# Kernel optimization log

Hardware: AMD Instinct MI355X
Metric: run time of the kernel (lower is better)

Reference implementation:

```python
import jax, jax.numpy as jnp
import numpy as np

N_NODES = 100000
N_EDGES = 20000  # hyperedges
NNZ = 800000
D = 128


def setup_inputs() -> dict:
    key = jax.random.key(0)
    ks = jax.random.split(key, 10)
    X = jax.random.normal(ks[0], (N_NODES, D), dtype=jnp.float32)
    X0 = jax.random.normal(ks[1], (N_NODES, D), dtype=jnp.float32)
    degE = jax.random.uniform(ks[2], (N_EDGES, 1), dtype=jnp.float32)
    degV = jax.random.uniform(ks[3], (N_NODES, 1), dtype=jnp.float32)
    alpha = jax.random.uniform(ks[4], (1,), dtype=jnp.float32)
    beta = jax.random.uniform(ks[5], (1,), dtype=jnp.float32)
    W_w = jax.random.normal(ks[6], (D, D), dtype=jnp.float32) / np.sqrt(D)
    g1_src = jax.random.randint(ks[7], (NNZ,), 0, N_NODES, dtype=jnp.int64 if jax.config.read('jax_enable_x64') else jnp.int32)
    g1_dst = jax.random.randint(ks[8], (NNZ,), 0, N_EDGES)
    g2_src = jax.random.randint(ks[9], (NNZ,), 0, N_EDGES)
    g2_dst = jax.random.randint(jax.random.fold_in(key, 99), (NNZ,), 0, N_NODES)
    return {"X": X, "X0": X0, "degE": degE, "degV": degV, "alpha": alpha,
            "beta": beta, "W_w": W_w, "g1_src": g1_src, "g1_dst": g1_dst,
            "g2_src": g2_src, "g2_dst": g2_dst}


def reference(X, X0, degE, degV, alpha, beta, W_w, g1_src, g1_dst, g2_src, g2_dst):
    n_edges = degE.shape[0]
    n_nodes = degV.shape[0]
    a = alpha[0]
    b = beta[0]
    # copy_u_sum(g1, X): gather node rows, scatter-sum into hyperedges
    Xe = jax.ops.segment_sum(X[g1_src], g1_dst, num_segments=n_edges)  # [E, D]
    Xe = Xe * degE
    # copy_u_sum(g2, Xe): gather hyperedge rows, scatter-sum into nodes
    Xv = jax.ops.segment_sum(Xe[g2_src], g2_dst, num_segments=n_nodes)  # [N, D]
    Xv = Xv * degV
    # GCNII-style initial residual + identity mapping
    Xi = (1.0 - a) * Xv + a * X0
    out = (1.0 - b) * Xi + b * (Xi @ W_w.T)  # Linear(bias=False)
    return out
```

## Files before the change

kernel.cpp:

```cpp
#include <hip/hip_runtime.h>

#define DD 128
#define SCAN_CHUNK 2048
#define PAD1 16
#define PAD2 8

typedef __attribute__((ext_vector_type(8))) _Float16 f16x8;
typedef __attribute__((ext_vector_type(4))) _Float16 f16x4;
typedef __attribute__((ext_vector_type(4))) float f32x4;

__global__ __launch_bounds__(256)
void k_hist1(const int* __restrict__ g1d, int* __restrict__ cnt1p,
             int* __restrict__ rank1, int nnz, int no, int hb,
             const float* __restrict__ W, const float* __restrict__ betaP,
             _Float16* __restrict__ Mh,
             const float* __restrict__ X, _Float16* __restrict__ Xh, int nx) {
    const int b = blockIdx.x;
    if (b < hb) {
        int q = b * 256 + threadIdx.x;
        if (q >= no) return;
        int i = q << 3;
        if (i + 8 <= nnz) {
            int4 d0 = *(const int4*)(g1d + i);
            int4 d1 = *(const int4*)(g1d + i + 4);
            int r0 = atomicAdd(&cnt1p[d0.x * PAD1], 1);
            int r1 = atomicAdd(&cnt1p[d0.y * PAD1], 1);
            int r2 = atomicAdd(&cnt1p[d0.z * PAD1], 1);
            int r3 = atomicAdd(&cnt1p[d0.w * PAD1], 1);
            int r4 = atomicAdd(&cnt1p[d1.x * PAD1], 1);
            int r5 = atomicAdd(&cnt1p[d1.y * PAD1], 1);
            int r6 = atomicAdd(&cnt1p[d1.z * PAD1], 1);
            int r7 = atomicAdd(&cnt1p[d1.w * PAD1], 1);
            *(int4*)(rank1 + i)     = make_int4(r0, r1, r2, r3);
            *(int4*)(rank1 + i + 4) = make_int4(r4, r5, r6, r7);
        } else {
            for (; i < nnz; ++i) rank1[i] = atomicAdd(&cnt1p[g1d[i] * PAD1], 1);
        }
        return;
    }
    if (b < hb + 8) {
        int gid = (b - hb) * 256 + threadIdx.x;
        if (gid >= DD * DD / 8) return;
        int c  = gid >> 4;
        int k0 = (gid & 15) << 3;
        float bb = betaP[0], ib = 1.0f - bb;
        const float* p = W + c * DD + k0;
        float4 lo = *(const float4*)p, hi = *(const float4*)(p + 4);
        float v[8] = {lo.x, lo.y, lo.z, lo.w, hi.x, hi.y, hi.z, hi.w};
        f16x8 t;
        #pragma unroll
        for (int j = 0; j < 8; ++j) {
            float m = bb * v[j] + ((k0 + j) == c ? ib : 0.0f);
            t[j] = (_Float16)m;
        }
        *(f16x8*)(Mh + (size_t)c * DD + k0) = t;
        return;
    }
    int gid = (b - hb - 8) * 256 + threadIdx.x;
    int i = gid << 3;
    if (i + 8 <= nx) {
        float4 lo = *(const float4*)(X + i);
        float4 hi = *(const float4*)(X + i + 4);
        f16x8 t;
        t[0] = (_Float16)lo.x; t[1] = (_Float16)lo.y;
        t[2] = (_Float16)lo.z; t[3] = (_Float16)lo.w;
        t[4] = (_Float16)hi.x; t[5] = (_Float16)hi.y;
        t[6] = (_Float16)hi.z; t[7] = (_Float16)hi.w;
        *(f16x8*)(Xh + i) = t;
    } else {
        for (; i < nx; ++i) Xh[i] = (_Float16)X[i];
    }
}

__global__ __launch_bounds__(256)
void k_scan_blocks(const int* __restrict__ cnt, int* __restrict__ off,
                   int* __restrict__ bsum, int n, int str) {
    __shared__ int sh[256];
    const int tid = threadIdx.x;
    const int base = blockIdx.x * SCAN_CHUNK + tid * 8;
    int v[8];
    int s = 0;
    #pragma unroll
    for (int j = 0; j < 8; ++j) {
        int idx = base + j;
        v[j] = (idx < n) ? cnt[(size_t)idx * str] : 0;
        s += v[j];
    }
    sh[tid] = s;
    __syncthreads();
    for (int d = 1; d < 256; d <<= 1) {
        int y = (tid >= d) ? sh[tid - d] : 0;
        __syncthreads();
        sh[tid] += y;
        __syncthreads();
    }
    int incl = sh[tid];
    int run = incl - s;
    #pragma unroll
    for (int j = 0; j < 8; ++j) {
        int idx = base + j;
        if (idx <= n) off[idx] = run;
        run += v[j];
    }
    if (tid == 255) bsum[blockIdx.x] = incl;
}

__global__ __launch_bounds__(256)
void k_fill(const int* __restrict__ dst, const int* __restrict__ src,
            const int* __restrict__ off, const int* __restrict__ rank,
            const int* __restrict__ bsum, int nb,
            int* __restrict__ out, int nnz) {
    __shared__ int pref[64];
    if (threadIdx.x == 0) {
        int run = 0;
        for (int i = 0; i < nb; ++i) { pref[i] = run; run += bsum[i]; }
        pref[nb] = run;
    }
    __syncthreads();
    int q = blockIdx.x * 256 + threadIdx.x;
    int i = q << 2;
    if (i + 4 <= nnz) {
        int4 d = *(const int4*)(dst + i);
        int4 s = *(const int4*)(src + i);
        int4 r = *(const int4*)(rank + i);
        int o0 = off[d.x] + pref[d.x >> 11];
        int o1 = off[d.y] + pref[d.y >> 11];
        int o2 = off[d.z] + pref[d.z >> 11];
        int o3 = off[d.w] + pref[d.w >> 11];
        out[o0 + r.x] = s.x;
        out[o1 + r.y] = s.y;
        out[o2 + r.z] = s.z;
        out[o3 + r.w] = s.w;
    } else {
        for (; i < nnz; ++i)
            out[off[dst[i]] + pref[dst[i] >> 11] + rank[i]] = src[i];
    }
}

__global__ __launch_bounds__(256)
void k_h2_egather(const int* __restrict__ g2d, int* __restrict__ cnt2p,
                  int* __restrict__ rank2, int nnz, int no, int H,
                  const _Float16* __restrict__ Xh, const int* __restrict__ off1,
                  const int* __restrict__ bsum1, int nb1,
                  const int* __restrict__ srcs1, const float* __restrict__ degE,
                  _Float16* __restrict__ XeH, int n_edges) {
    if (blockIdx.x < H) {
        int q = blockIdx.x * 256 + threadIdx.x;
        if (q >= no) return;
        int i = q << 3;
        if (i + 8 <= nnz) {
            int4 d0 = *(const int4*)(g2d + i);
            int4 d1 = *(const int4*)(g2d + i + 4);
            int r0 = atomicAdd(&cnt2p[d0.x * PAD2], 1);
            int r1 = atomicAdd(&cnt2p[d0.y * PAD2], 1);
            int r2 = atomicAdd(&cnt2p[d0.z * PAD2], 1);
            int r3 = atomicAdd(&cnt2p[d0.w * PAD2], 1);
            int r4 = atomicAdd(&cnt2p[d1.x * PAD2], 1);
            int r5 = atomicAdd(&cnt2p[d1.y * PAD2], 1);
            int r6 = atomicAdd(&cnt2p[d1.z * PAD2], 1);
            int r7 = atomicAdd(&cnt2p[d1.w * PAD2], 1);
            *(int4*)(rank2 + i)     = make_int4(r0, r1, r2, r3);
            *(int4*)(rank2 + i + 4) = make_int4(r4, r5, r6, r7);
        } else {
            for (; i < nnz; ++i) rank2[i] = atomicAdd(&cnt2p[g2d[i] * PAD2], 1);
        }
        return;
    }
    __shared__ int pref[16];
    if (threadIdx.x == 0) {
        int run = 0;
        for (int i = 0; i < nb1; ++i) { pref[i] = run; run += bsum1[i]; }
        pref[nb1] = run;
    }
    __syncthreads();
    const int wid  = threadIdx.x >> 6;
    const int lane = threadIdx.x & 63;
    int e = (blockIdx.x - H) * 4 + wid;
    if (e >= n_edges) return;
    const int g = lane >> 4;
    const int c = lane & 15;
    int beg = off1[e] + pref[e >> 11];
    int end = off1[e + 1] + pref[(e + 1) >> 11];
    float a0[8] = {0, 0, 0, 0, 0, 0, 0, 0};
    float a1[8] = {0, 0, 0, 0, 0, 0, 0, 0};
    int j = beg + g;
    for (; j + 4 < end; j += 8) {
        int s0 = srcs1[j];
        int s1 = srcs1[j + 4];
        f16x8 v0 = *(const f16x8*)(Xh + (size_t)s0 * DD + c * 8);
        f16x8 v1 = *(const f16x8*)(Xh + (size_t)s1 * DD + c * 8);
        #pragma unroll
        for (int t = 0; t < 8; ++t) { a0[t] += (float)v0[t]; a1[t] += (float)v1[t]; }
    }
    if (j < end) {
        int s = srcs1[j];
        f16x8 v = *(const f16x8*)(Xh + (size_t)s * DD + c * 8);
        #pragma unroll
        for (int t = 0; t < 8; ++t) a0[t] += (float)v[t];
    }
    float r[8];
    #pragma unroll
    for (int t = 0; t < 8; ++t) r[t] = a0[t] + a1[t];
    #pragma unroll
    for (int t = 0; t < 8; ++t) r[t] += __shfl_xor(r[t], 16);
    #pragma unroll
    for (int t = 0; t < 8; ++t) r[t] += __shfl_xor(r[t], 32);
    if (g == 0) {
        float f = degE[e];
        f16x8 ob;
        #pragma unroll
        for (int t = 0; t < 8; ++t) ob[t] = (_Float16)(f * r[t]);
        *(f16x8*)(XeH + (size_t)e * DD + c * 8) = ob;
    }
}

__global__ __launch_bounds__(256)
void k_ng_gemm(const _Float16* __restrict__ XeH, const int* __restrict__ off2,
               const int* __restrict__ bsum2, int nb2,
               const int* __restrict__ srcs2, const float* __restrict__ degV,
               const float* __restrict__ X0, const float* __restrict__ alphaP,
               const _Float16* __restrict__ Mh, float* __restrict__ out,
               int n_nodes) {
    __shared__ int pref[64];
    __shared__ _Float16 xi_lds[4][16 * DD];
    const int tid = threadIdx.x;
    if (tid == 0) {
        int run = 0;
        for (int i = 0; i < nb2; ++i) { pref[i] = run; run += bsum2[i]; }
        pref[nb2] = run;
    }
    __syncthreads();
    const int wid  = tid >> 6;
    const int lane = tid & 63;
    const int strip = blockIdx.x * 4 + wid;
    const int row0 = strip * 16;
    const bool live = row0 < n_nodes;
    _Float16* lbase = &xi_lds[wid][0];

    const int r16 = lane >> 2;
    const int sl  = lane & 3;
    const int row = row0 + r16;
    if (live) {
        float acc[32];
        #pragma unroll
        for (int t = 0; t < 32; ++t) acc[t] = 0.0f;
        if (row < n_nodes) {
            int beg = off2[row] + pref[row >> 11];
            int end = off2[row + 1] + pref[(row + 1) >> 11];
            int j = beg;
            for (; j + 2 <= end; j += 2) {
                int s0 = srcs2[j];
                int s1 = srcs2[j + 1];
                const _Float16* p0 = XeH + (size_t)s0 * DD + sl * 32;
                const _Float16* p1 = XeH + (size_t)s1 * DD + sl * 32;
                f16x8 u0 = *(const f16x8*)(p0);
                f16x8 u1 = *(const f16x8*)(p0 + 8);
                f16x8 u2 = *(const f16x8*)(p0 + 16);
                f16x8 u3 = *(const f16x8*)(p0 + 24);
                f16x8 w0 = *(const f16x8*)(p1);
                f16x8 w1 = *(const f16x8*)(p1 + 8);
                f16x8 w2 = *(const f16x8*)(p1 + 16);
                f16x8 w3 = *(const f16x8*)(p1 + 24);
                #pragma unroll
                for (int t = 0; t < 8; ++t) {
                    acc[t]      += (float)u0[t] + (float)w0[t];
                    acc[8 + t]  += (float)u1[t] + (float)w1[t];
                    acc[16 + t] += (float)u2[t] + (float)w2[t];
                    acc[24 + t] += (float)u3[t] + (float)w3[t];
                }
            }
            if (j < end) {
                int s = srcs2[j];
                const _Float16* p0 = XeH + (size_t)s * DD + sl * 32;
                f16x8 u0 = *(const f16x8*)(p0);
                f16x8 u1 = *(const f16x8*)(p0 + 8);
                f16x8 u2 = *(const f16x8*)(p0 + 16);
                f16x8 u3 = *(const f16x8*)(p0 + 24);
                #pragma unroll
                for (int t = 0; t < 8; ++t) {
                    acc[t]      += (float)u0[t];
                    acc[8 + t]  += (float)u1[t];
                    acc[16 + t] += (float)u2[t];
                    acc[24 + t] += (float)u3[t];
                }
            }
            float a = alphaP[0];
            float f = (1.0f - a) * degV[row];
            const float* x0p = X0 + (size_t)row * DD + sl * 32;
            #pragma unroll
            for (int c2 = 0; c2 < 4; ++c2) {
                float4 xa = *(const float4*)(x0p + c2 * 8);
                float4 xb = *(const float4*)(x0p + c2 * 8 + 4);
                f16x8 h;
                h[0] = (_Float16)(f * acc[c2 * 8 + 0] + a * xa.x);
                h[1] = (_Float16)(f * acc[c2 * 8 + 1] + a * xa.y);
                h[2] = (_Float16)(f * acc[c2 * 8 + 2] + a * xa.z);
                h[3] = (_Float16)(f * acc[c2 * 8 + 3] + a * xa.w);
                h[4] = (_Float16)(f * acc[c2 * 8 + 4] + a * xb.x);
                h[5] = (_Float16)(f * acc[c2 * 8 + 5] + a * xb.y);
                h[6] = (_Float16)(f * acc[c2 * 8 + 6] + a * xb.z);
                h[7] = (_Float16)(f * acc[c2 * 8 + 7] + a * xb.w);
                int byte = r16 * 256 + sl * 64 + c2 * 16;
                byte ^= (r16 & 7) << 4;
                *(f16x8*)((char*)lbase + byte) = h;
            }
        } else {
            f16x8 z = {0, 0, 0, 0, 0, 0, 0, 0};
            #pragma unroll
            for (int c2 = 0; c2 < 4; ++c2) {
                int byte = r16 * 256 + sl * 64 + c2 * 16;
                byte ^= (r16 & 7) << 4;
                *(f16x8*)((char*)lbase + byte) = z;
            }
        }
    }
    __syncthreads();
    if (!live) return;

    const int m16  = lane & 15;
    const int quad = lane >> 4;
    const int kq   = quad * 8;
    f16x8 af[4];
    #pragma unroll
    for (int kf = 0; kf < 4; ++kf) {
        int byte = m16 * 256 + kf * 64 + quad * 16;
        byte ^= (m16 & 7) << 4;
        af[kf] = *(const f16x8*)((const char*)lbase + byte);
    }
    #pragma unroll
    for (int nt = 0; nt < 8; ++nt) {
        const _Float16* mr = Mh + (size_t)(nt * 16 + m16) * DD + kq;
        f32x4 acc = {0.f, 0.f, 0.f, 0.f};
        #pragma unroll
        for (int kf = 0; kf < 4; ++kf) {
            f16x8 bfrag = *(const f16x8*)(mr + kf * 32);
            acc = __builtin_amdgcn_mfma_f32_16x16x32_f16(af[kf], bfrag, acc, 0, 0, 0);
        }
        const int col = nt * 16 + m16;
        #pragma unroll
        for (int r = 0; r < 4; ++r) {
            int orow = row0 + quad * 4 + r;
            if (orow < n_nodes)
                out[(size_t)orow * DD + col] = acc[r];
        }
    }
}

extern "C" void kernel_launch(void* const* d_in, const int* in_sizes, int n_in,
                              void* d_out, int out_size, void* d_ws, size_t ws_size,
                              hipStream_t stream) {
    const float* X     = (const float*)d_in[0];
    const float* X0    = (const float*)d_in[1];
    const float* degE  = (const float*)d_in[2];
    const float* degV  = (const float*)d_in[3];
    const float* alpha = (const float*)d_in[4];
    const float* beta  = (const float*)d_in[5];
    const float* W     = (const float*)d_in[6];
    const int*   g1s   = (const int*)d_in[7];
    const int*   g1d   = (const int*)d_in[8];
    const int*   g2s   = (const int*)d_in[9];
    const int*   g2d   = (const int*)d_in[10];
    float* out = (float*)d_out;

    const int n_nodes = in_sizes[3];
    const int n_edges = in_sizes[2];
    const int nnz     = in_sizes[7];
    const int nx      = n_nodes * DD;

    int*   wsi   = (int*)d_ws;
    _Float16* XeH = (_Float16*)d_ws;
    size_t o     = (size_t)n_edges * DD / 2;
    int*   rank1 = wsi + o;
    int*   rank2 = rank1;
    o += nnz;
    int*   off1  = wsi + o;          o += n_edges + 1;
    int*   off2  = wsi + o;          o += n_nodes + 1;
    size_t srcs_base = o;
    int*   srcs1 = wsi + o;          o += nnz;
    int*   srcs2 = wsi + o;          o += nnz;
    int*   bsum  = wsi + o;          o += 128;
    _Float16* Mh = (_Float16*)(wsi + o); o += DD * DD / 2;
    int*   cnt1p = wsi + srcs_base;
    int*   cnt2p = wsi + srcs_base + nnz;
    _Float16* Xh = (_Float16*)d_out;

    hipMemsetAsync(cnt1p, 0, 2 * (size_t)nnz * sizeof(int), stream);

    const int nb1 = (n_edges + SCAN_CHUNK - 1) / SCAN_CHUNK;
    const int nb2 = (n_nodes + SCAN_CHUNK - 1) / SCAN_CHUNK;
    const int no  = (nnz + 7) / 8;
    const int hb  = (no + 255) / 256;
    const int cb  = (nx / 8 + 255) / 256;
    const int nq  = (nnz + 3) / 4;
    const int qb  = (nq + 255) / 256;

    k_hist1<<<hb + 8 + cb, 256, 0, stream>>>(g1d, cnt1p, rank1, nnz, no, hb,
                                             W, beta, Mh, X, Xh, nx);
    k_scan_blocks<<<nb1, 256, 0, stream>>>(cnt1p, off1, bsum, n_edges, PAD1);
    k_fill<<<qb, 256, 0, stream>>>(g1d, g1s, off1, rank1, bsum, nb1, srcs1, nnz);

    const int egb = (n_edges + 3) / 4;
    k_h2_egather<<<hb + egb, 256, 0, stream>>>(g2d, cnt2p, rank2, nnz, no, hb,
                                               Xh, off1, bsum, nb1,
                                               srcs1, degE, XeH, n_edges);

    k_scan_blocks<<<nb2, 256, 0, stream>>>(cnt2p, off2, bsum + 64, n_nodes, PAD2);
    k_fill<<<qb, 256, 0, stream>>>(g2d, g2s, off2, rank2, bsum + 64, nb2, srcs2, nnz);

    const int nstrips = (n_nodes + 15) / 16;
    k_ng_gemm<<<(nstrips + 3) / 4, 256, 0, stream>>>(
        XeH, off2, bsum + 64, nb2, srcs2, degV, X0, alpha, Mh, out, n_nodes);
}
```

Baseline: 354.6 us.

## Remap node gather to 16 lanes per row, split GEMM across waves, parallelize prefix

The node-gather/GEMM kernel now gives each 256-thread block one 16-row strip. Each row is served by 16 lanes that each gather 16 bytes, instead of 4 lanes gathering 64 bytes, and the 8 MFMA column tiles are split across the 4 waves instead of being computed per wave. The edge gather unrolls to 4 outstanding loads per lane, and the per-block prefix of block sums is loaded in parallel into LDS instead of by one thread reading global memory serially. This aims to raise memory-level parallelism and coalescing in the irregular gathers. The cost is 4x more blocks and the per-block prefix setup plus a barrier repeated in each of them.

```diff
diff --git a/kernel.cpp b/kernel.cpp
--- a/kernel.cpp
+++ b/kernel.cpp
@@ -45,8 +45,8 @@
         int k0 = (gid & 15) << 3;
         float bb = betaP[0], ib = 1.0f - bb;
         const float* p = W + c * DD + k0;
-        float4 lo = *(const float4*)p, hi = *(const float4*)(p + 4);
-        float v[8] = {lo.x, lo.y, lo.z, lo.w, hi.x, hi.y, hi.z, hi.w};
+        f32x4 lo = *(const f32x4*)p, hi = *(const f32x4*)(p + 4);
+        float v[8] = {lo[0], lo[1], lo[2], lo[3], hi[0], hi[1], hi[2], hi[3]};
         f16x8 t;
         #pragma unroll
         for (int j = 0; j < 8; ++j) {
@@ -59,13 +59,13 @@
     int gid = (b - hb - 8) * 256 + threadIdx.x;
     int i = gid << 3;
     if (i + 8 <= nx) {
-        float4 lo = *(const float4*)(X + i);
-        float4 hi = *(const float4*)(X + i + 4);
+        f32x4 lo = *(const f32x4*)(X + i);
+        f32x4 hi = *(const f32x4*)(X + i + 4);
         f16x8 t;
-        t[0] = (_Float16)lo.x; t[1] = (_Float16)lo.y;
-        t[2] = (_Float16)lo.z; t[3] = (_Float16)lo.w;
-        t[4] = (_Float16)hi.x; t[5] = (_Float16)hi.y;
-        t[6] = (_Float16)hi.z; t[7] = (_Float16)hi.w;
+        t[0] = (_Float16)lo[0]; t[1] = (_Float16)lo[1];
+        t[2] = (_Float16)lo[2]; t[3] = (_Float16)lo[3];
+        t[4] = (_Float16)hi[0]; t[5] = (_Float16)hi[1];
+        t[6] = (_Float16)hi[2]; t[7] = (_Float16)hi[3];
         *(f16x8*)(Xh + i) = t;
     } else {
         for (; i < nx; ++i) Xh[i] = (_Float16)X[i];
@@ -105,18 +105,25 @@
     if (tid == 255) bsum[blockIdx.x] = incl;
 }
 
+__device__ __forceinline__ void lds_pref(int* pref, const int* bsum, int nb,
+                                         int tid) {
+    if (tid < 64) pref[tid] = (tid < nb) ? bsum[tid] : 0;
+    __syncthreads();
+    if (tid == 0) {
+        int run = 0;
+        for (int i = 0; i < nb; ++i) { int t = pref[i]; pref[i] = run; run += t; }
+        pref[nb] = run;
+    }
+    __syncthreads();
+}
+
 __global__ __launch_bounds__(256)
 void k_fill(const int* __restrict__ dst, const int* __restrict__ src,
             const int* __restrict__ off, const int* __restrict__ rank,
             const int* __restrict__ bsum, int nb,
             int* __restrict__ out, int nnz) {
-    __shared__ int pref[64];
-    if (threadIdx.x == 0) {
-        int run = 0;
-        for (int i = 0; i < nb; ++i) { pref[i] = run; run += bsum[i]; }
-        pref[nb] = run;
-    }
-    __syncthreads();
+    __shared__ int pref[65];
+    lds_pref(pref, bsum, nb, threadIdx.x);
     int q = blockIdx.x * 256 + threadIdx.x;
     int i = q << 2;
     if (i + 4 <= nnz) {
@@ -166,13 +173,8 @@
         }
         return;
     }
-    __shared__ int pref[16];
-    if (threadIdx.x == 0) {
-        int run = 0;
-        for (int i = 0; i < nb1; ++i) { pref[i] = run; run += bsum1[i]; }
-        pref[nb1] = run;
-    }
-    __syncthreads();
+    __shared__ int pref[17];
+    lds_pref(pref, bsum1, nb1, threadIdx.x);
     const int wid  = threadIdx.x >> 6;
     const int lane = threadIdx.x & 63;
     int e = (blockIdx.x - H) * 4 + wid;
@@ -184,15 +186,22 @@
     float a0[8] = {0, 0, 0, 0, 0, 0, 0, 0};
     float a1[8] = {0, 0, 0, 0, 0, 0, 0, 0};
     int j = beg + g;
-    for (; j + 4 < end; j += 8) {
+    for (; j + 12 < end; j += 16) {
         int s0 = srcs1[j];
         int s1 = srcs1[j + 4];
+        int s2 = srcs1[j + 8];
+        int s3 = srcs1[j + 12];
         f16x8 v0 = *(const f16x8*)(Xh + (size_t)s0 * DD + c * 8);
         f16x8 v1 = *(const f16x8*)(Xh + (size_t)s1 * DD + c * 8);
-        #pragma unroll
-        for (int t = 0; t < 8; ++t) { a0[t] += (float)v0[t]; a1[t] += (float)v1[t]; }
-    }
-    if (j < end) {
+        f16x8 v2 = *(const f16x8*)(Xh + (size_t)s2 * DD + c * 8);
+        f16x8 v3 = *(const f16x8*)(Xh + (size_t)s3 * DD + c * 8);
+        #pragma unroll
+        for (int t = 0; t < 8; ++t) {
+            a0[t] += (float)v0[t] + (float)v2[t];
+            a1[t] += (float)v1[t] + (float)v3[t];
+        }
+    }
+    for (; j < end; j += 4) {
         int s = srcs1[j];
         f16x8 v = *(const f16x8*)(Xh + (size_t)s * DD + c * 8);
         #pragma unroll
@@ -221,101 +230,71 @@
                const float* __restrict__ X0, const float* __restrict__ alphaP,
                const _Float16* __restrict__ Mh, float* __restrict__ out,
                int n_nodes) {
-    __shared__ int pref[64];
-    __shared__ _Float16 xi_lds[4][16 * DD];
+    __shared__ int pref[65];
+    __shared__ _Float16 xi_lds[16 * DD];
     const int tid = threadIdx.x;
-    if (tid == 0) {
-        int run = 0;
-        for (int i = 0; i < nb2; ++i) { pref[i] = run; run += bsum2[i]; }
-        pref[nb2] = run;
-    }
-    __syncthreads();
+    lds_pref(pref, bsum2, nb2, tid);
     const int wid  = tid >> 6;
     const int lane = tid & 63;
-    const int strip = blockIdx.x * 4 + wid;
-    const int row0 = strip * 16;
-    const bool live = row0 < n_nodes;
-    _Float16* lbase = &xi_lds[wid][0];
-
-    const int r16 = lane >> 2;
-    const int sl  = lane & 3;
-    const int row = row0 + r16;
-    if (live) {
-        float acc[32];
-        #pragma unroll
-        for (int t = 0; t < 32; ++t) acc[t] = 0.0f;
+    const int g    = lane >> 4;
+    const int c    = lane & 15;
+    const int r16  = wid * 4 + g;
+    const int row0 = blockIdx.x * 16;
+    const int row  = row0 + r16;
+
+    {
+        float a0[8] = {0, 0, 0, 0, 0, 0, 0, 0};
+        float a1[8] = {0, 0, 0, 0, 0, 0, 0, 0};
         if (row < n_nodes) {
             int beg = off2[row] + pref[row >> 11];
             int end = off2[row + 1] + pref[(row + 1) >> 11];
             int j = beg;
-            for (; j + 2 <= end; j += 2) {
+            for (; j + 3 < end; j += 4) {
                 int s0 = srcs2[j];
                 int s1 = srcs2[j + 1];
-                const _Float16* p0 = XeH + (size_t)s0 * DD + sl * 32;
-                const _Float16* p1 = XeH + (size_t)s1 * DD + sl * 32;
-                f16x8 u0 = *(const f16x8*)(p0);
-                f16x8 u1 = *(const f16x8*)(p0 + 8);
-                f16x8 u2 = *(const f16x8*)(p0 + 16);
-                f16x8 u3 = *(const f16x8*)(p0 + 24);
-                f16x8 w0 = *(const f16x8*)(p1);
-                f16x8 w1 = *(const f16x8*)(p1 + 8);
-                f16x8 w2 = *(const f16x8*)(p1 + 16);
-                f16x8 w3 = *(const f16x8*)(p1 + 24);
+                int s2 = srcs2[j + 2];
+                int s3 = srcs2[j + 3];
+                f16x8 v0 = *(const f16x8*)(XeH + (size_t)s0 * DD + c * 8);
+                f16x8 v1 = *(const f16x8*)(XeH + (size_t)s1 * DD + c * 8);
+                f16x8 v2 = *(const f16x8*)(XeH + (size_t)s2 * DD + c * 8);
+                f16x8 v3 = *(const f16x8*)(XeH + (size_t)s3 * DD + c * 8);
                 #pragma unroll
                 for (int t = 0; t < 8; ++t) {
-                    acc[t]      += (float)u0[t] + (float)w0[t];
-                    acc[8 + t]  += (float)u1[t] + (float)w1[t];
-                    acc[16 + t] += (float)u2[t] + (float)w2[t];
-                    acc[24 + t] += (float)u3[t] + (float)w3[t];
+                    a0[t] += (float)v0[t] + (float)v2[t];
+                    a1[t] += (float)v1[t] + (float)v3[t];
                 }
             }
-            if (j < end) {
+            for (; j < end; ++j) {
                 int s = srcs2[j];
-                const _Float16* p0 = XeH + (size_t)s * DD + sl * 32;
-                f16x8 u0 = *(const f16x8*)(p0);
-                f16x8 u1 = *(const f16x8*)(p0 + 8);
-                f16x8 u2 = *(const f16x8*)(p0 + 16);
-                f16x8 u3 = *(const f16x8*)(p0 + 24);
+                f16x8 v = *(const f16x8*)(XeH + (size_t)s * DD + c * 8);
                 #pragma unroll
-                for (int t = 0; t < 8; ++t) {
-                    acc[t]      += (float)u0[t];
-                    acc[8 + t]  += (float)u1[t];
-                    acc[16 + t] += (float)u2[t];
-                    acc[24 + t] += (float)u3[t];
-                }
+                for (int t = 0; t < 8; ++t) a0[t] += (float)v[t];
             }
             float a = alphaP[0];
             float f = (1.0f - a) * degV[row];
-            const float* x0p = X0 + (size_t)row * DD + sl * 32;
-            #pragma unroll
-            for (int c2 = 0; c2 < 4; ++c2) {
-                float4 xa = *(const float4*)(x0p + c2 * 8);
-                float4 xb = *(const float4*)(x0p + c2 * 8 + 4);
-                f16x8 h;
-                h[0] = (_Float16)(f * acc[c2 * 8 + 0] + a * xa.x);
-                h[1] = (_Float16)(f * acc[c2 * 8 + 1] + a * xa.y);
-                h[2] = (_Float16)(f * acc[c2 * 8 + 2] + a * xa.z);
-                h[3] = (_Float16)(f * acc[c2 * 8 + 3] + a * xa.w);
-                h[4] = (_Float16)(f * acc[c2 * 8 + 4] + a * xb.x);
-                h[5] = (_Float16)(f * acc[c2 * 8 + 5] + a * xb.y);
-                h[6] = (_Float16)(f * acc[c2 * 8 + 6] + a * xb.z);
-                h[7] = (_Float16)(f * acc[c2 * 8 + 7] + a * xb.w);
-                int byte = r16 * 256 + sl * 64 + c2 * 16;
-                byte ^= (r16 & 7) << 4;
-                *(f16x8*)((char*)lbase + byte) = h;
-            }
+            const float* x0p = X0 + (size_t)row * DD + c * 8;
+            f32x4 xa = *(const f32x4*)(x0p);
+            f32x4 xb = *(const f32x4*)(x0p + 4);
+            f16x8 h;
+            h[0] = (_Float16)(f * (a0[0] + a1[0]) + a * xa[0]);
+            h[1] = (_Float16)(f * (a0[1] + a1[1]) + a * xa[1]);
+            h[2] = (_Float16)(f * (a0[2] + a1[2]) + a * xa[2]);
+            h[3] = (_Float16)(f * (a0[3] + a1[3]) + a * xa[3]);
+            h[4] = (_Float16)(f * (a0[4] + a1[4]) + a * xb[0]);
+            h[5] = (_Float16)(f * (a0[5] + a1[5]) + a * xb[1]);
+            h[6] = (_Float16)(f * (a0[6] + a1[6]) + a * xb[2]);
+            h[7] = (_Float16)(f * (a0[7] + a1[7]) + a * xb[3]);
+            int byte = r16 * 256 + c * 16;
+            byte ^= (r16 & 7) << 4;
+            *(f16x8*)((char*)xi_lds + byte) = h;
         } else {
             f16x8 z = {0, 0, 0, 0, 0, 0, 0, 0};
-            #pragma unroll
-            for (int c2 = 0; c2 < 4; ++c2) {
-                int byte = r16 * 256 + sl * 64 + c2 * 16;
-                byte ^= (r16 & 7) << 4;
-                *(f16x8*)((char*)lbase + byte) = z;
-            }
+            int byte = r16 * 256 + c * 16;
+            byte ^= (r16 & 7) << 4;
+            *(f16x8*)((char*)xi_lds + byte) = z;
         }
     }
     __syncthreads();
-    if (!live) return;
 
     const int m16  = lane & 15;
     const int quad = lane >> 4;
@@ -325,18 +304,19 @@
     for (int kf = 0; kf < 4; ++kf) {
         int byte = m16 * 256 + kf * 64 + quad * 16;
         byte ^= (m16 & 7) << 4;
-        af[kf] = *(const f16x8*)((const char*)lbase + byte);
-    }
-    #pragma unroll
-    for (int nt = 0; nt < 8; ++nt) {
-        const _Float16* mr = Mh + (size_t)(nt * 16 + m16) * DD + kq;
+        af[kf] = *(const f16x8*)((const char*)xi_lds + byte);
+    }
+    #pragma unroll
+    for (int u = 0; u < 2; ++u) {
+        const int nt2 = wid * 2 + u;
+        const _Float16* mr = Mh + (size_t)(nt2 * 16 + m16) * DD + kq;
         f32x4 acc = {0.f, 0.f, 0.f, 0.f};
         #pragma unroll
         for (int kf = 0; kf < 4; ++kf) {
             f16x8 bfrag = *(const f16x8*)(mr + kf * 32);
             acc = __builtin_amdgcn_mfma_f32_16x16x32_f16(af[kf], bfrag, acc, 0, 0, 0);
         }
-        const int col = nt * 16 + m16;
+        const int col = nt2 * 16 + m16;
         #pragma unroll
         for (int r = 0; r < 4; ++r) {
             int orow = row0 + quad * 4 + r;
@@ -408,6 +388,6 @@
     k_fill<<<qb, 256, 0, stream>>>(g2d, g2s, off2, rank2, bsum + 64, nb2, srcs2, nnz);
 
     const int nstrips = (n_nodes + 15) / 16;
-    k_ng_gemm<<<(nstrips + 3) / 4, 256, 0, stream>>>(
+    k_ng_gemm<<<nstrips, 256, 0, stream>>>(
         XeH, off2, bsum + 64, nb2, srcs2, degV, X0, alpha, Mh, out, n_nodes);
 }
```

New measurement: 341.1 us. -3.8%, faster.
